# Kernel tuning notes

Measured on AMD Instinct MI355X. Metric: run time of the kernel, lower is better.

Reference implementation:

```python
import jax, jax.numpy as jnp
import numpy as np
from jax import lax

ULB_LEN = 50000  # hardcoded ulb_dest_len in Cluster.__init__
EPS = 1e-8       # torch.cosine_similarity eps


def _l2norm(x):
    n = jnp.sqrt(jnp.sum(x * x, axis=-1, keepdims=True))
    return x / jnp.maximum(n, EPS)


def setup_inputs() -> dict:
    key = jax.random.key(0)
    k1, k2, k3, k4, k5 = jax.random.split(key, 5)
    B, C, D, K = 32768, 1000, 256, 16
    return {
        "feature": jax.random.normal(k1, (B, D), dtype=jnp.float32),
        "pred": jax.random.normal(k2, (B, C), dtype=jnp.float32),
        "centroids": jax.random.normal(k3, (C, D), dtype=jnp.float32),
        "pred_top_N": jax.random.uniform(k4, (C, K), dtype=jnp.float32),
        "unlabeled_index": jax.random.randint(k5, (B,), 0, ULB_LEN, dtype=jnp.int64),
    }


def reference(feature, pred, centroids, pred_top_N, unlabeled_index):
    B = feature.shape[0]
    C, K = pred_top_N.shape

    # batched cosine similarity to centroids -> argmax label, max cos
    cos = _l2norm(feature) @ _l2norm(centroids).T          # [B, C]
    label = jnp.argmax(cos, axis=1)                        # [B]
    cos_f = jnp.max(cos, axis=1)                           # [B]

    # confidence scores from softmax(pred)
    scores = jnp.max(jax.nn.softmax(pred, axis=1), axis=1)  # [B]

    # per-class mean / unbiased variance of cos_f (torch.var default unbiased)
    ones = jnp.ones((B,), dtype=cos_f.dtype)
    cnt = jax.ops.segment_sum(ones, label, num_segments=C)
    s1 = jax.ops.segment_sum(cos_f, label, num_segments=C)
    s2 = jax.ops.segment_sum(cos_f * cos_f, label, num_segments=C)
    mean = s1 / jnp.maximum(cnt, 1.0)
    var = (s2 - cnt * mean * mean) / jnp.maximum(cnt - 1.0, 1.0)
    std = jnp.sqrt(jnp.maximum(var, 0.0) + 1e-12)

    # weight[i] = normal(mean, std).pdf(cos_f[i]) if cos_f[i] < mean[label] else 1
    m_i, s_i = mean[label], std[label]
    inv_sqrt_2pi = 1.0 / jnp.sqrt(2.0 * jnp.pi).astype(cos_f.dtype)
    pdf = jnp.exp(-0.5 * ((cos_f - m_i) / s_i) ** 2) * inv_sqrt_2pi / s_i
    weight = jnp.where(cos_f < m_i, pdf, jnp.ones_like(cos_f))

    # sequential top-N scatter-insert into pred_top_N / fake_index
    fake_index = jnp.full((C, K), -1, dtype=jnp.int32)

    def step(carry, xs):
        topN, fidx = carry
        lb, sc, ui = xs
        row = topN[lb]                       # [K]
        mi = jnp.argmin(row)
        mv = row[mi]
        do = sc > mv
        topN = topN.at[lb, mi].set(jnp.where(do, sc, mv))
        fidx = fidx.at[lb, mi].set(jnp.where(do, ui.astype(jnp.int32), fidx[lb, mi]))
        return (topN, fidx), None

    (topN, fidx), _ = lax.scan(
        step, (pred_top_N, fake_index),
        (label, scores, unlabeled_index))

    # selected_label scatter (all samples selected: select==1 everywhere)
    selected_label = jnp.full((ULB_LEN,), -1, dtype=jnp.int32)
    selected_label = selected_label.at[unlabeled_index].set(label.astype(jnp.int32))

    return label.astype(jnp.float32), weight, topN, fidx, selected_label
```

## Files before the change

### kernel.cpp

```cpp
#include <hip/hip_runtime.h>
#include <cstdint>
#include <cstddef>

#define B_N   32768
#define C_N   1000
#define C_PAD 1024
#define D_N   256
#define K_N   16
#define ULB_N 50000
#define NCHUNK 128
#define CAP_L 128

#define OFF_L 0
#define OFF_W 32768
#define OFF_T 65536
#define OFF_F 81536
#define OFF_S 97536

typedef __attribute__((ext_vector_type(8))) short short8;
typedef __attribute__((ext_vector_type(4))) float f32x4;

__device__ __forceinline__ unsigned ordf(float f) {
  unsigned u = __float_as_uint(f);
  return (u & 0x80000000u) ? ~u : (u | 0x80000000u);
}
__device__ __forceinline__ float iordf(unsigned h) {
  unsigned u = (h & 0x80000000u) ? (h & 0x7FFFFFFFu) : ~h;
  return __uint_as_float(u);
}
__device__ __forceinline__ unsigned short f2bf(float f) {
  unsigned u = __float_as_uint(f);
  return (unsigned short)((u + 0x7FFFu + ((u >> 16) & 1u)) >> 16);
}
__device__ __forceinline__ float bf2f(unsigned short h) {
  return __uint_as_float(((unsigned)h) << 16);
}

__device__ __forceinline__ void pack_body(const float* __restrict__ src,
                                          short8* __restrict__ dst,
                                          int mtL, int mt0, int nreal) {
  __shared__ float s[16][260];
  __shared__ float part[16][16];
  __shared__ float dv[16];
  const int t = threadIdx.x;
  const int r = t >> 4, c4 = (t & 15) * 4;
  const int grow = (mt0 + mtL) * 16 + r;
  #pragma unroll
  for (int i = 0; i < 4; ++i) {
    float4 v;
    if (grow < nreal) v = *reinterpret_cast<const float4*>(&src[(size_t)grow * D_N + c4 + 64 * i]);
    else { v.x = 0.f; v.y = 0.f; v.z = 0.f; v.w = 0.f; }
    s[r][c4 + 64 * i + 0] = v.x; s[r][c4 + 64 * i + 1] = v.y;
    s[r][c4 + 64 * i + 2] = v.z; s[r][c4 + 64 * i + 3] = v.w;
  }
  __syncthreads();
  {
    int c0 = t & 15;
    float ss = 0.f;
    #pragma unroll
    for (int j = 0; j < 16; ++j) { float x = s[r][c0 + 16 * j]; ss += x * x; }
    part[r][c0] = ss;
  }
  __syncthreads();
  if (t < 16) {
    float ss = 0.f;
    #pragma unroll
    for (int j = 0; j < 16; ++j) ss += part[t][j];
    dv[t] = 1.0f / fmaxf(sqrtf(ss), 1e-8f);
  }
  __syncthreads();
  #pragma unroll
  for (int i = 0; i < 4; ++i) {
    int p = t + 256 * i;
    int si = p >> 6, l = p & 63;
    int mr = l & 15, g = l >> 4;
    int kc = (si & 7) * 32 + g * 8;
    bool lo = si >= 8;
    float di = dv[mr];
    short8 v;
    #pragma unroll
    for (int j = 0; j < 8; ++j) {
      float q = s[mr][kc + j] * di;
      unsigned short hi = f2bf(q);
      unsigned short e = lo ? f2bf(q - bf2f(hi)) : hi;
      v[j] = (short)e;
    }
    dst[(size_t)mtL * 1024 + p] = v;
  }
  __syncthreads();
}

__global__ __launch_bounds__(256) void k_front(const float* __restrict__ cent,
                                               const float* __restrict__ pred,
                                               const float* __restrict__ feat,
                                               short8* __restrict__ Bp,
                                               short8* __restrict__ Ap,
                                               int packA,
                                               float* __restrict__ scores,
                                               unsigned long long* keys, float* s1, float* s2,
                                               int* cnt, int* besti) {
  __shared__ float red[8];
  int i = blockIdx.x * blockDim.x + threadIdx.x;
  if (i < B_N)  keys[i] = 0ull;
  if (i < C_PAD) { s1[i] = 0.f; s2[i] = 0.f; cnt[i] = 0; }
  if (i < ULB_N) besti[i] = -1;
  if (blockIdx.x < 64) pack_body(cent, Bp, blockIdx.x, 0, C_N);
  if (packA && blockIdx.x < 2048) pack_body(feat, Ap, blockIdx.x, 0, B_N);

  int r = blockIdx.x, t = threadIdx.x;
  const float* row = pred + (size_t)r * C_N;
  float4 v;
  bool act = t < 250;
  if (act) v = *reinterpret_cast<const float4*>(&row[t * 4]);
  else { v.x = -INFINITY; v.y = -INFINITY; v.z = -INFINITY; v.w = -INFINITY; }
  float m = fmaxf(fmaxf(v.x, v.y), fmaxf(v.z, v.w));
  #pragma unroll
  for (int mk = 1; mk < 64; mk <<= 1) m = fmaxf(m, __shfl_xor(m, mk, 64));
  int wid = t >> 6, lane = t & 63;
  if (lane == 0) red[wid] = m;
  __syncthreads();
  m = fmaxf(fmaxf(red[0], red[1]), fmaxf(red[2], red[3]));
  float s = act ? expf(v.x - m) + expf(v.y - m) + expf(v.z - m) + expf(v.w - m) : 0.f;
  #pragma unroll
  for (int mk = 1; mk < 64; mk <<= 1) s += __shfl_xor(s, mk, 64);
  __syncthreads();
  if (lane == 0) red[4 + wid] = s;
  __syncthreads();
  if (t == 0) {
    float S = ((red[4] + red[5]) + red[6]) + red[7];
    scores[r] = 1.0f / S;
  }
}

__global__ __launch_bounds__(256) void k_pack(const float* __restrict__ src,
                                              short8* __restrict__ dst,
                                              int mt0, int nreal) {
  pack_body(src, dst, blockIdx.x, mt0, nreal);
}

__global__ __launch_bounds__(256, 2) void k_mfma(const short8* __restrict__ Ap,
                                                 const short8* __restrict__ Bp,
                                                 unsigned long long* __restrict__ keys,
                                                 int row0) {
  const int bid = blockIdx.x;
  const int nby = gridDim.x >> 3;
  int byl, bx;
  if ((nby & 63) == 0) {
    int xcd = bid & 7, j = bid >> 3;
    int slab = nby >> 3;
    int grp = j >> 6, jj = j & 63;
    byl = xcd * slab + grp * 8 + (jj & 7);
    bx = jj >> 3;
  } else { byl = bid >> 3; bx = bid & 7; }

  const int w = threadIdx.x >> 6, l = threadIdx.x & 63;
  const int wm = (w & 1) * 64, wn = (w >> 1) * 64;
  const short8* a0 = Ap + (size_t)(byl * 8 + (wm >> 4)) * 1024 + l;
  const short8* b0 = Bp + (size_t)(bx * 8 + (wn >> 4)) * 1024 + l;

  f32x4 acc[4][4];
  #pragma unroll
  for (int i = 0; i < 4; ++i)
    #pragma unroll
    for (int j = 0; j < 4; ++j) { acc[i][j][0] = 0.f; acc[i][j][1] = 0.f; acc[i][j][2] = 0.f; acc[i][j][3] = 0.f; }

  short8 A0h[4], B0h[4], A0l[4], B0l[4];
  short8 A1h[4], B1h[4], A1l[4], B1l[4];
#define LOADSET(Xh, Yh, Xl, Yl, ks) { \
    _Pragma("unroll") \
    for (int i = 0; i < 4; ++i) Xh[i] = a0[(ks) * 64 + i * 1024]; \
    _Pragma("unroll") \
    for (int i = 0; i < 4; ++i) Yh[i] = b0[(ks) * 64 + i * 1024]; \
    _Pragma("unroll") \
    for (int i = 0; i < 4; ++i) Xl[i] = a0[((ks) + 8) * 64 + i * 1024]; \
    _Pragma("unroll") \
    for (int i = 0; i < 4; ++i) Yl[i] = b0[((ks) + 8) * 64 + i * 1024]; }
#define MFMA16(fa, fb) { \
    _Pragma("unroll") \
    for (int mi = 0; mi < 4; ++mi) \
      _Pragma("unroll") \
      for (int nj = 0; nj < 4; ++nj) \
        acc[mi][nj] = __builtin_amdgcn_mfma_f32_16x16x32_bf16(fa[mi], fb[nj], acc[mi][nj], 0, 0, 0); }
#define MFMA48(Xh, Yh, Xl, Yl) { MFMA16(Xh, Yh) MFMA16(Xl, Yh) MFMA16(Xh, Yl) }
#define FENCE __builtin_amdgcn_sched_barrier(0);

  LOADSET(A0h, B0h, A0l, B0l, 0)
  #pragma unroll 1
  for (int ks = 0; ks < 6; ks += 2) {
    LOADSET(A1h, B1h, A1l, B1l, ks + 1)
    FENCE
    MFMA48(A0h, B0h, A0l, B0l)
    FENCE
    LOADSET(A0h, B0h, A0l, B0l, ks + 2)
    FENCE
    MFMA48(A1h, B1h, A1l, B1l)
    FENCE
  }
  LOADSET(A1h, B1h, A1l, B1l, 7)
  FENCE
  MFMA48(A0h, B0h, A0l, B0l)
  FENCE
  MFMA48(A1h, B1h, A1l, B1l)
#undef LOADSET
#undef MFMA16
#undef MFMA48
#undef FENCE

  const int cb = bx * 128 + wn + (l & 15);
  #pragma unroll
  for (int mi = 0; mi < 4; ++mi) {
    #pragma unroll
    for (int r = 0; r < 4; ++r) {
      float bv = -INFINITY; int bc = 0x7FFFFFFF;
      #pragma unroll
      for (int nj = 0; nj < 4; ++nj) {
        int c = cb + nj * 16;
        float v = acc[mi][nj][r];
        if (c < C_N && v > bv) { bv = v; bc = c; }
      }
      #pragma unroll
      for (int mk = 1; mk < 16; mk <<= 1) {
        float ov = __shfl_xor(bv, mk, 64);
        int oc = __shfl_xor(bc, mk, 64);
        if (ov > bv || (ov == bv && oc < bc)) { bv = ov; bc = oc; }
      }
      if ((l & 15) == 0) {
        unsigned long long kk =
            (((unsigned long long)ordf(bv)) << 32) |
            (unsigned long long)(0xFFFFFFFFu - (unsigned)bc);
        atomicMax(&keys[row0 + byl * 128 + wm + mi * 16 + (l >> 4) * 4 + r], kk);
      }
    }
  }
}

__global__ __launch_bounds__(256) void k_post(const unsigned long long* __restrict__ keys,
                                              const int* __restrict__ ui,
                                              int* __restrict__ labels, float* __restrict__ cosf_,
                                              float* __restrict__ s1, float* __restrict__ s2,
                                              int* __restrict__ cnt, int* __restrict__ besti,
                                              unsigned short* __restrict__ lrank,
                                              unsigned short* __restrict__ hist,
                                              float* __restrict__ out) {
  __shared__ int lab[256];
  __shared__ unsigned histl[C_PAD];
  int chunk = blockIdx.x, t = threadIdx.x;
  int b = chunk * 256 + t;
  #pragma unroll
  for (int r = 0; r < 4; ++r) histl[t + 256 * r] = 0;
  unsigned long long k = keys[b];
  int c = (int)(0xFFFFFFFFu - (unsigned)k);
  float f = iordf((unsigned)(k >> 32));
  labels[b] = c;
  cosf_[b] = f;
  out[OFF_L + b] = (float)c;
  atomicAdd(&s1[c], f);
  atomicAdd(&s2[c], f * f);
  atomicAdd(&cnt[c], 1);
  atomicMax(&besti[ui[b]], b);
  lab[t] = c;
  __syncthreads();
  atomicAdd(&histl[c], 1u);
  unsigned rk = 0;
  for (int j = 0; j < t; ++j) rk += (lab[j] == c);
  lrank[b] = (unsigned short)rk;
  __syncthreads();
  #pragma unroll
  for (int r = 0; r < 4; ++r)
    hist[chunk * C_PAD + t + 256 * r] = (unsigned short)histl[t + 256 * r];
}

__global__ __launch_bounds__(256) void k_prefix(const unsigned short* __restrict__ hist,
                                                unsigned short* __restrict__ base,
                                                int* __restrict__ class_n) {
  int c = blockIdx.x * 4 + (threadIdx.x >> 6);
  int l = threadIdx.x & 63;
  unsigned h0 = hist[(2 * l) * C_PAD + c];
  unsigned h1 = hist[(2 * l + 1) * C_PAD + c];
  unsigned pair = h0 + h1;
  unsigned s = pair;
  #pragma unroll
  for (int off = 1; off < 64; off <<= 1) {
    unsigned v = __shfl_up(s, off, 64);
    if (l >= off) s += v;
  }
  unsigned excl = s - pair;
  base[(2 * l) * C_PAD + c] = (unsigned short)excl;
  base[(2 * l + 1) * C_PAD + c] = (unsigned short)(excl + h0);
  if (l == 63) class_n[c] = (int)s;
}

__global__ __launch_bounds__(256) void k_sw(const int* __restrict__ labels,
                                            const unsigned short* __restrict__ lrank,
                                            const unsigned short* __restrict__ base,
                                            const float* __restrict__ scores,
                                            const int* __restrict__ ui,
                                            const float* __restrict__ cosf_,
                                            const float* __restrict__ s1,
                                            const float* __restrict__ s2,
                                            const int* __restrict__ cnt,
                                            const int* __restrict__ besti,
                                            float* __restrict__ lists_s,
                                            int* __restrict__ lists_u,
                                            float* __restrict__ out) {
  int b = blockIdx.x * blockDim.x + threadIdx.x;
  if (b >= B_N) return;
  int c = labels[b];
  int chunk = b >> 8;
  int pos = (int)base[chunk * C_PAD + c] + (int)lrank[b];
  if (pos < CAP_L) {
    lists_s[c * CAP_L + pos] = scores[b];
    lists_u[c * CAP_L + pos] = ui[b];
  }
  float n = (float)cnt[c];
  float m = s1[c] / fmaxf(n, 1.0f);
  float var = (s2[c] - n * m * m) / fmaxf(n - 1.0f, 1.0f);
  float sd = sqrtf(fmaxf(var, 0.0f) + 1e-12f);
  float cf = cosf_[b];
  float wgt = 1.0f;
  if (cf < m) {
    float z = (cf - m) / sd;
    const float inv = 0.3989422804014327f;
    wgt = expf(-0.5f * (z * z)) * inv / sd;
  }
  out[OFF_W + b] = wgt;
  {
    int bi = besti[b];
    out[OFF_S + b] = (bi < 0) ? -1.0f : (float)labels[bi];
  }
  int p2 = b + B_N;
  if (p2 < ULB_N) {
    int bi = besti[p2];
    out[OFF_S + p2] = (bi < 0) ? -1.0f : (float)labels[bi];
  }
}

__global__ __launch_bounds__(256) void k_replay(const float* __restrict__ ptn,
                                                const float* __restrict__ lists_s,
                                                const int* __restrict__ lists_u,
                                                const int* __restrict__ class_n,
                                                const int* __restrict__ labels,
                                                const float* __restrict__ scores,
                                                const int* __restrict__ ui,
                                                float* __restrict__ out) {
  int c = blockIdx.x * 4 + (threadIdx.x >> 6);
  int lane = threadIdx.x & 63;
  if (c >= C_N) return;

  float tv[K_N]; int fi[K_N];
  #pragma unroll
  for (int j = 0; j < K_N; ++j) { tv[j] = ptn[c * K_N + j]; fi[j] = -1; }

  auto ins = [&](float s, int u) {
    float mv = tv[0]; int mi = 0;
    #pragma unroll
    for (int j = 1; j < K_N; ++j) { if (tv[j] < mv) { mv = tv[j]; mi = j; } }
    if (s > mv) {
      #pragma unroll
      for (int j = 0; j < K_N; ++j) { if (j == mi) { tv[j] = s; fi[j] = u; } }
    }
  };

  int n = class_n[c];
  if (n <= CAP_L) {
    for (int t0 = 0; t0 < n; t0 += 64) {
      float s = 0.f; int u = 0;
      int idx = t0 + lane;
      if (idx < n) { s = lists_s[c * CAP_L + idx]; u = lists_u[c * CAP_L + idx]; }
      int lim = min(64, n - t0);
      for (int t = 0; t < lim; ++t) {
        float ss = __shfl(s, t, 64);
        int uu = __shfl(u, t, 64);
        ins(ss, uu);
      }
    }
  } else {
    for (int t0 = 0; t0 < B_N; t0 += 64) {
      int lb = labels[t0 + lane];
      unsigned long long match = __ballot(lb == c);
      while (match) {
        int t = __ffsll((long long)match) - 1;
        match &= match - 1;
        int b = t0 + t;
        ins(scores[b], ui[b]);
      }
    }
  }

  if (lane == 0) {
    #pragma unroll
    for (int j = 0; j < K_N; ++j) {
      out[OFF_T + c * K_N + j] = tv[j];
      out[OFF_F + c * K_N + j] = (float)fi[j];
    }
  }
}

extern "C" void kernel_launch(void* const* d_in, const int* in_sizes, int n_in,
                              void* d_out, int out_size, void* d_ws, size_t ws_size,
                              hipStream_t stream) {
  const float* feat = (const float*)d_in[0];
  const float* pred = (const float*)d_in[1];
  const float* cent = (const float*)d_in[2];
  const float* ptn  = (const float*)d_in[3];
  const int*   ui   = (const int*)d_in[4];
  float* out = (float*)d_out;
  char* ws = (char*)d_ws;

  size_t o = 0;
  auto alloc = [&](size_t bytes) { void* p = ws + o; o += (bytes + 255) & ~size_t(255); return p; };
  short8* Bp                = (short8*)alloc(64 * 1024 * 16);
  unsigned long long* keys  = (unsigned long long*)alloc(B_N * 8);
  int*   labels             = (int*)  alloc(B_N * 4);
  float* scores             = (float*)alloc(B_N * 4);
  float* cosf_              = (float*)alloc(B_N * 4);
  float* s1                 = (float*)alloc(C_PAD * 4);
  float* s2                 = (float*)alloc(C_PAD * 4);
  int*   cnt                = (int*)  alloc(C_PAD * 4);
  int*   besti              = (int*)  alloc(ULB_N * 4);
  unsigned short* lrank     = (unsigned short*)alloc(B_N * 2);
  unsigned short* hist      = (unsigned short*)alloc(NCHUNK * C_PAD * 2);
  unsigned short* base      = (unsigned short*)alloc(NCHUNK * C_PAD * 2);
  int*   class_n            = (int*)  alloc(C_PAD * 4);
  float* lists_s            = (float*)alloc(C_N * CAP_L * 4);
  int*   lists_u            = (int*)  alloc(C_N * CAP_L * 4);

  size_t avail = (ws_size > o) ? ws_size - o : 0;
  int g128 = (int)(avail / 131072ull);
  if (g128 < 1) g128 = 1;
  if (g128 > 256) g128 = 256;
  if (g128 >= 64) g128 &= ~63;
  else if (g128 >= 8) g128 &= ~7;
  short8* Achunk = (short8*)(ws + o);
  int fullA = (g128 >= 256) ? 1 : 0;

  k_front    <<<B_N, 256, 0, stream>>>(cent, pred, feat, Bp, Achunk, fullA, scores, keys, s1, s2, cnt, besti);
  if (fullA) {
    k_mfma   <<<2048, 256, 0, stream>>>(Achunk, Bp, keys, 0);
  } else {
    for (int c0 = 0; c0 < 256; c0 += g128) {
      int g = (g128 < 256 - c0) ? g128 : (256 - c0);
      k_pack <<<g * 8, 256, 0, stream>>>(feat, Achunk, c0 * 8, B_N);
      k_mfma <<<g * 8, 256, 0, stream>>>(Achunk, Bp, keys, c0 * 128);
    }
  }
  k_post     <<<NCHUNK, 256, 0, stream>>>(keys, ui, labels, cosf_, s1, s2, cnt, besti, lrank, hist, out);
  k_prefix   <<<256, 256, 0, stream>>>(hist, base, class_n);
  k_sw       <<<B_N / 256, 256, 0, stream>>>(labels, lrank, base, scores, ui, cosf_, s1, s2, cnt, besti, lists_s, lists_u, out);
  k_replay   <<<250, 256, 0, stream>>>(ptn, lists_s, lists_u, class_n, labels, scores, ui, out);
}
```

Measured before the change: 148.0 us.

## Move softmax score computation into MFMA kernel tail and shrink front grid

The row-wise softmax max/sum over pred moves out of the 32768-block front kernel. It now runs as a tail step in the MFMA kernel, handled by the bx==0 blocks, one wave per row. The front kernel launches only 2048 blocks to zero buffers and pack operands. This cuts the large launch and overlaps the memory-bound pred read with compute-bound matrix work. In exchange, only 1/8 of the MFMA blocks carry the extra pred reads, which creates load imbalance at the tail.

```diff
diff --git a/kernel.cpp b/kernel.cpp
--- a/kernel.cpp
+++ b/kernel.cpp
@@ -91,22 +91,29 @@
 }
 
 __global__ __launch_bounds__(256) void k_front(const float* __restrict__ cent,
-                                               const float* __restrict__ pred,
                                                const float* __restrict__ feat,
                                                short8* __restrict__ Bp,
                                                short8* __restrict__ Ap,
                                                int packA,
-                                               float* __restrict__ scores,
                                                unsigned long long* keys, float* s1, float* s2,
                                                int* cnt, int* besti) {
-  __shared__ float red[8];
   int i = blockIdx.x * blockDim.x + threadIdx.x;
   if (i < B_N)  keys[i] = 0ull;
   if (i < C_PAD) { s1[i] = 0.f; s2[i] = 0.f; cnt[i] = 0; }
   if (i < ULB_N) besti[i] = -1;
   if (blockIdx.x < 64) pack_body(cent, Bp, blockIdx.x, 0, C_N);
-  if (packA && blockIdx.x < 2048) pack_body(feat, Ap, blockIdx.x, 0, B_N);
-
+  if (packA) pack_body(feat, Ap, blockIdx.x, 0, B_N);
+}
+
+__global__ __launch_bounds__(256) void k_pack(const float* __restrict__ src,
+                                              short8* __restrict__ dst,
+                                              int mt0, int nreal) {
+  pack_body(src, dst, blockIdx.x, mt0, nreal);
+}
+
+__global__ __launch_bounds__(256) void k_scores(const float* __restrict__ pred,
+                                                float* __restrict__ scores) {
+  __shared__ float red[8];
   int r = blockIdx.x, t = threadIdx.x;
   const float* row = pred + (size_t)r * C_N;
   float4 v;
@@ -132,16 +139,12 @@
   }
 }
 
-__global__ __launch_bounds__(256) void k_pack(const float* __restrict__ src,
-                                              short8* __restrict__ dst,
-                                              int mt0, int nreal) {
-  pack_body(src, dst, blockIdx.x, mt0, nreal);
-}
-
 __global__ __launch_bounds__(256, 2) void k_mfma(const short8* __restrict__ Ap,
                                                  const short8* __restrict__ Bp,
+                                                 const float* __restrict__ pred,
+                                                 float* __restrict__ scores,
                                                  unsigned long long* __restrict__ keys,
-                                                 int row0) {
+                                                 int row0, int doScores) {
   const int bid = blockIdx.x;
   const int nby = gridDim.x >> 3;
   int byl, bx;
@@ -230,6 +233,33 @@
             (unsigned long long)(0xFFFFFFFFu - (unsigned)bc);
         atomicMax(&keys[row0 + byl * 128 + wm + mi * 16 + (l >> 4) * 4 + r], kk);
       }
+    }
+  }
+
+  if (doScores && bx == 0) {
+    const int rbase = row0 + byl * 128;
+    for (int rr = w; rr < 128; rr += 4) {
+      const float* row = pred + (size_t)(rbase + rr) * C_N;
+      float4 v[4];
+      float mx = -INFINITY;
+      #pragma unroll
+      for (int j = 0; j < 4; ++j) {
+        int p = l + 64 * j;
+        if (p < 250) v[j] = *reinterpret_cast<const float4*>(&row[p * 4]);
+        else { v[j].x = -INFINITY; v[j].y = -INFINITY; v[j].z = -INFINITY; v[j].w = -INFINITY; }
+        mx = fmaxf(mx, fmaxf(fmaxf(v[j].x, v[j].y), fmaxf(v[j].z, v[j].w)));
+      }
+      #pragma unroll
+      for (int mk = 1; mk < 64; mk <<= 1) mx = fmaxf(mx, __shfl_xor(mx, mk, 64));
+      float s = 0.f;
+      #pragma unroll
+      for (int j = 0; j < 4; ++j) {
+        if (l + 64 * j < 250)
+          s += expf(v[j].x - mx) + expf(v[j].y - mx) + expf(v[j].z - mx) + expf(v[j].w - mx);
+      }
+      #pragma unroll
+      for (int mk = 1; mk < 64; mk <<= 1) s += __shfl_xor(s, mk, 64);
+      if (l == 0) scores[rbase + rr] = 1.0f / s;
     }
   }
 }
@@ -434,14 +464,15 @@
   short8* Achunk = (short8*)(ws + o);
   int fullA = (g128 >= 256) ? 1 : 0;
 
-  k_front    <<<B_N, 256, 0, stream>>>(cent, pred, feat, Bp, Achunk, fullA, scores, keys, s1, s2, cnt, besti);
+  k_front    <<<2048, 256, 0, stream>>>(cent, feat, Bp, Achunk, fullA, keys, s1, s2, cnt, besti);
   if (fullA) {
-    k_mfma   <<<2048, 256, 0, stream>>>(Achunk, Bp, keys, 0);
+    k_mfma   <<<2048, 256, 0, stream>>>(Achunk, Bp, pred, scores, keys, 0, 1);
   } else {
+    k_scores <<<B_N, 256, 0, stream>>>(pred, scores);
     for (int c0 = 0; c0 < 256; c0 += g128) {
       int g = (g128 < 256 - c0) ? g128 : (256 - c0);
       k_pack <<<g * 8, 256, 0, stream>>>(feat, Achunk, c0 * 8, B_N);
-      k_mfma <<<g * 8, 256, 0, stream>>>(Achunk, Bp, keys, c0 * 128);
+      k_mfma <<<g * 8, 256, 0, stream>>>(Achunk, Bp, pred, scores, keys, c0 * 128, 0);
     }
   }
   k_post     <<<NCHUNK, 256, 0, stream>>>(keys, ui, labels, cosf_, s1, s2, cnt, besti, lrank, hist, out);
```

Result: slower. 160.3 us (+8.3%).
